# Kernel tuning notes

Hardware: AMD Instinct MI355X
Metric: run time of the kernel (lower is better)

## Reference

```python
import jax, jax.numpy as jnp
import numpy as np

N = 8192
MARGIN = 0.01
PRICE_W = 0.5
RANK_W = 0.5


def setup_inputs() -> dict:
    key = jax.random.key(0)
    k1, k2, k3 = jax.random.split(key, 3)
    predicted_prices = jax.random.normal(k1, (N,), dtype=jnp.float32)
    actual_prices = jax.random.normal(k2, (N,), dtype=jnp.float32)
    # keep previous prices in [0.5, 1.5) so the division is well-behaved
    previous_prices = jax.random.uniform(k3, (N,), dtype=jnp.float32) + 0.5
    return {"predicted_prices": predicted_prices,
            "actual_prices": actual_prices,
            "previous_prices": previous_prices}


def reference(predicted_prices, actual_prices, previous_prices):
    # MSE price loss
    price_loss = jnp.mean((predicted_prices - actual_prices) ** 2)

    pred_r = (predicted_prices - previous_prices) / previous_prices  # [N]
    act_r = (actual_prices - previous_prices) / previous_prices     # [N]

    # pairwise differences (i, j): r[i] - r[j]
    act_diff = act_r[:, None] - act_r[None, :]      # [N, N]
    pred_diff = pred_r[:, None] - pred_r[None, :]   # [N, N]

    n = pred_r.shape[0]
    upper = jnp.triu(jnp.ones((n, n), dtype=bool), k=1)  # j > i
    valid = upper & (act_diff != 0)

    # margin_ranking_loss(x1=pred_diff, x2=0, target=sign(act_diff)):
    #   max(0, -target * pred_diff + margin)
    hinge = jnp.maximum(0.0, -jnp.sign(act_diff) * pred_diff + MARGIN)

    count = jnp.sum(valid)
    rank_sum = jnp.sum(jnp.where(valid, hinge, 0.0))
    ranking_loss = jnp.where(
        count > 0,
        rank_sum / jnp.maximum(count, 1).astype(hinge.dtype),
        jnp.zeros((), dtype=hinge.dtype),
    )

    total_loss = PRICE_W * price_loss + RANK_W * ranking_loss
    return total_loss
```

## Files before the change

kernel.cpp:

```cpp
#include <hip/hip_runtime.h>

constexpr int    NN     = 8192;
constexpr float  MARGIN = 0.01f;
constexpr int    BT     = 256;
constexpr int    FI     = 4;
constexpr int    TI     = BT * FI;
constexpr int    TJ     = 32;
constexpr int    NTI    = NN / TI;
constexpr int    NTJ    = NN / TJ;
constexpr int    NBLOCKS = 8 * 256 - 32 * 28;

__global__ __launch_bounds__(BT)
void pair_kernel(const float* __restrict__ pred,
                 const float* __restrict__ act,
                 const float* __restrict__ prev,
                 double* __restrict__ partials)
{
    int t  = blockIdx.x;
    int ib = 0;
    while (t >= NTJ - 32 * ib) { t -= NTJ - 32 * ib; ++ib; }
    const int  jc        = 32 * ib + t;
    const bool diag_like = (t < 32);
    const bool do_price  = (t == 0);

    __shared__ alignas(16) float2 s_t[TJ];

    const int tid = threadIdx.x;
    if (tid < TJ) {
        const int   j   = jc * TJ + tid;
        const float pv  = prev[j];
        const float rcp = __builtin_amdgcn_rcpf(pv);
        s_t[tid] = make_float2((pred[j] - pv) * rcp, (act[j] - pv) * rcp);
    }

    float pri[FI], ari[FI];
    double pp = 0.0;
#pragma unroll
    for (int f = 0; f < FI; ++f) {
        const int   i   = ib * TI + f * BT + tid;
        const float pv  = prev[i];
        const float p   = pred[i];
        const float a   = act[i];
        const float rcp = __builtin_amdgcn_rcpf(pv);
        pri[f] = (p - pv) * rcp;
        ari[f] = (a - pv) * rcp;
        if (do_price) {
            const float d = p - a;
            pp += (double)(d * d);
        }
    }

    __syncthreads();

    float acc[FI] = {0.f, 0.f, 0.f, 0.f};

#define PAIR(f, pj, aj)                                     \
    {                                                       \
        const float ad = ari[f] - (aj);                     \
        const float pd = pri[f] - (pj);                     \
        const float s  = (ad > 0.0f) ? -1.0f : 1.0f;        \
        acc[f] += fmaxf(0.0f, fmaf(s, pd, MARGIN));         \
    }

    const float4* __restrict__ s4 = (const float4*)s_t;
#pragma unroll
    for (int g = 0; g < TJ / 2; ++g) {
        const float4 q = s4[g];
        PAIR(0, q.x, q.y); PAIR(1, q.x, q.y);
        PAIR(2, q.x, q.y); PAIR(3, q.x, q.y);
        PAIR(0, q.z, q.w); PAIR(1, q.z, q.w);
        PAIR(2, q.z, q.w); PAIR(3, q.z, q.w);
    }
#undef PAIR

    double ws = (double)((acc[0] + acc[1]) + (acc[2] + acc[3]));
    if (!diag_like) ws += ws;

    for (int off = 32; off > 0; off >>= 1) {
        ws += __shfl_down(ws, off, 64);
        pp += __shfl_down(pp, off, 64);
    }

    __shared__ double rs[4], rp[4];
    const int w = tid >> 6;
    if ((tid & 63) == 0) { rs[w] = ws; rp[w] = pp; }
    __syncthreads();
    if (tid == 0) {
        partials[2 * blockIdx.x + 0] = rs[0] + rs[1] + rs[2] + rs[3];
        partials[2 * blockIdx.x + 1] = rp[0] + rp[1] + rp[2] + rp[3];
    }
}

__global__ __launch_bounds__(256)
void finalize_kernel(const double* __restrict__ partials,
                     float* __restrict__ out)
{
    double s = 0.0, p = 0.0;
    for (int t = threadIdx.x; t < NBLOCKS; t += 256) {
        s += partials[2 * t + 0];
        p += partials[2 * t + 1];
    }
    for (int off = 32; off > 0; off >>= 1) {
        s += __shfl_down(s, off, 64);
        p += __shfl_down(p, off, 64);
    }
    __shared__ double rs[4], rp[4];
    const int w = threadIdx.x >> 6;
    if ((threadIdx.x & 63) == 0) { rs[w] = s; rp[w] = p; }
    __syncthreads();
    if (threadIdx.x == 0) {
        const double S = rs[0] + rs[1] + rs[2] + rs[3];
        const double P = rp[0] + rp[1] + rp[2] + rp[3];
        const double rank = (S - (double)NN * (double)MARGIN)
                          / ((double)NN * (double)(NN - 1));
        out[0] = (float)(0.5 * (P / (double)NN) + 0.5 * rank);
    }
}

extern "C" void kernel_launch(void* const* d_in, const int* in_sizes, int n_in,
                              void* d_out, int out_size, void* d_ws, size_t ws_size,
                              hipStream_t stream)
{
    const float* pred = (const float*)d_in[0];
    const float* act  = (const float*)d_in[1];
    const float* prev = (const float*)d_in[2];

    double* partials = (double*)d_ws;

    pair_kernel<<<NBLOCKS, BT, 0, stream>>>(pred, act, prev, partials);
    finalize_kernel<<<1, 256, 0, stream>>>(partials, (float*)d_out);
}
```

Before: 14.75 us.

## Halve rows per thread, double block count, and reduce partials in float

Each thread now covers 2 i-rows instead of 4, so the triangular tiling uses 512-row i-blocks and roughly twice as many blocks, giving more parallelism across the CUs. The double-precision wave-shuffle reductions are replaced by a float shared-memory plus shuffle reduction, and rank and price partials are stored in separate float arrays, with the price partial written once per i-block. Each j-tile value loaded from LDS is now reused across fewer rows, per-block overhead rises, and summing in float may cost some accuracy.

```diff
diff --git a/kernel.cpp b/kernel.cpp
--- a/kernel.cpp
+++ b/kernel.cpp
@@ -3,27 +3,30 @@
 constexpr int    NN     = 8192;
 constexpr float  MARGIN = 0.01f;
 constexpr int    BT     = 256;
-constexpr int    FI     = 4;
+constexpr int    FI     = 2;
 constexpr int    TI     = BT * FI;
 constexpr int    TJ     = 32;
 constexpr int    NTI    = NN / TI;
 constexpr int    NTJ    = NN / TJ;
-constexpr int    NBLOCKS = 8 * 256 - 32 * 28;
+constexpr int    NBLOCKS = 16 * 256 - 16 * 120;
 
 __global__ __launch_bounds__(BT)
 void pair_kernel(const float* __restrict__ pred,
                  const float* __restrict__ act,
                  const float* __restrict__ prev,
-                 double* __restrict__ partials)
+                 float* __restrict__ rank_part,
+                 float* __restrict__ price_part)
 {
     int t  = blockIdx.x;
     int ib = 0;
-    while (t >= NTJ - 32 * ib) { t -= NTJ - 32 * ib; ++ib; }
-    const int  jc        = 32 * ib + t;
-    const bool diag_like = (t < 32);
+    while (t >= NTJ - 16 * ib) { t -= NTJ - 16 * ib; ++ib; }
+    const int  jc        = 16 * ib + t;
+    const bool diag_like = (t < 16);
     const bool do_price  = (t == 0);
 
     __shared__ alignas(16) float2 s_t[TJ];
+    __shared__ float s_red[BT];
+    __shared__ float s_pp[BT];
 
     const int tid = threadIdx.x;
     if (tid < TJ) {
@@ -34,7 +37,7 @@
     }
 
     float pri[FI], ari[FI];
-    double pp = 0.0;
+    float pp = 0.f;
 #pragma unroll
     for (int f = 0; f < FI; ++f) {
         const int   i   = ib * TI + f * BT + tid;
@@ -44,62 +47,58 @@
         const float rcp = __builtin_amdgcn_rcpf(pv);
         pri[f] = (p - pv) * rcp;
         ari[f] = (a - pv) * rcp;
-        if (do_price) {
-            const float d = p - a;
-            pp += (double)(d * d);
-        }
+        const float d = p - a;
+        pp += d * d;
     }
 
     __syncthreads();
 
-    float acc[FI] = {0.f, 0.f, 0.f, 0.f};
+    float acc[4] = {0.f, 0.f, 0.f, 0.f};
 
-#define PAIR(f, pj, aj)                                     \
+#define PAIR(f, k, pj, aj)                                  \
     {                                                       \
         const float ad = ari[f] - (aj);                     \
         const float pd = pri[f] - (pj);                     \
         const float s  = (ad > 0.0f) ? -1.0f : 1.0f;        \
-        acc[f] += fmaxf(0.0f, fmaf(s, pd, MARGIN));         \
+        acc[k] += fmaxf(0.0f, fmaf(s, pd, MARGIN));         \
     }
 
     const float4* __restrict__ s4 = (const float4*)s_t;
 #pragma unroll
     for (int g = 0; g < TJ / 2; ++g) {
         const float4 q = s4[g];
-        PAIR(0, q.x, q.y); PAIR(1, q.x, q.y);
-        PAIR(2, q.x, q.y); PAIR(3, q.x, q.y);
-        PAIR(0, q.z, q.w); PAIR(1, q.z, q.w);
-        PAIR(2, q.z, q.w); PAIR(3, q.z, q.w);
+        PAIR(0, 0, q.x, q.y); PAIR(1, 1, q.x, q.y);
+        PAIR(0, 2, q.z, q.w); PAIR(1, 3, q.z, q.w);
     }
 #undef PAIR
 
-    double ws = (double)((acc[0] + acc[1]) + (acc[2] + acc[3]));
-    if (!diag_like) ws += ws;
+    float w = (acc[0] + acc[1]) + (acc[2] + acc[3]);
+    if (!diag_like) w += w;
 
-    for (int off = 32; off > 0; off >>= 1) {
-        ws += __shfl_down(ws, off, 64);
-        pp += __shfl_down(pp, off, 64);
-    }
+    s_red[tid] = w;
+    s_pp[tid]  = pp;
+    __syncthreads();
 
-    __shared__ double rs[4], rp[4];
-    const int w = tid >> 6;
-    if ((tid & 63) == 0) { rs[w] = ws; rp[w] = pp; }
-    __syncthreads();
-    if (tid == 0) {
-        partials[2 * blockIdx.x + 0] = rs[0] + rs[1] + rs[2] + rs[3];
-        partials[2 * blockIdx.x + 1] = rp[0] + rp[1] + rp[2] + rp[3];
+    if (tid < 64) {
+        float r = s_red[tid] + s_red[tid + 64] + s_red[tid + 128] + s_red[tid + 192];
+        for (int off = 32; off > 0; off >>= 1) r += __shfl_down(r, off, 64);
+        if (tid == 0) rank_part[blockIdx.x] = r;
+        if (do_price) {
+            float q = s_pp[tid] + s_pp[tid + 64] + s_pp[tid + 128] + s_pp[tid + 192];
+            for (int off = 32; off > 0; off >>= 1) q += __shfl_down(q, off, 64);
+            if (tid == 0) price_part[ib] = q;
+        }
     }
 }
 
 __global__ __launch_bounds__(256)
-void finalize_kernel(const double* __restrict__ partials,
+void finalize_kernel(const float* __restrict__ rank_part,
+                     const float* __restrict__ price_part,
                      float* __restrict__ out)
 {
     double s = 0.0, p = 0.0;
-    for (int t = threadIdx.x; t < NBLOCKS; t += 256) {
-        s += partials[2 * t + 0];
-        p += partials[2 * t + 1];
-    }
+    for (int t = threadIdx.x; t < NBLOCKS; t += 256) s += (double)rank_part[t];
+    if (threadIdx.x < NTI) p = (double)price_part[threadIdx.x];
     for (int off = 32; off > 0; off >>= 1) {
         s += __shfl_down(s, off, 64);
         p += __shfl_down(p, off, 64);
@@ -125,8 +124,10 @@
     const float* act  = (const float*)d_in[1];
     const float* prev = (const float*)d_in[2];
 
-    double* partials = (double*)d_ws;
+    char* w = (char*)d_ws;
+    float* rank_part  = (float*)w;
+    float* price_part = (float*)(w + 12288);
 
-    pair_kernel<<<NBLOCKS, BT, 0, stream>>>(pred, act, prev, partials);
-    finalize_kernel<<<1, 256, 0, stream>>>(partials, (float*)d_out);
+    pair_kernel<<<NBLOCKS, BT, 0, stream>>>(pred, act, prev, rank_part, price_part);
+    finalize_kernel<<<1, 256, 0, stream>>>(rank_part, price_part, (float*)d_out);
 }
```

Result: slower. 15.31 us (+3.8%).

## Fuse finalize into pair kernel via last-block atomic counter, widen j tile

Applied to the files above, without the earlier changes.

Drops the separate finalize kernel. Each block writes a float partial and bumps an atomic counter, and the last block to finish does the final reduction. The j-tile grows from 32 to 64, which halves the block count, and per-block partials and the price sum now use float instead of double. A memset of the counter is added before the launch, and float partials may lose some accuracy.

```diff
diff --git a/kernel.cpp b/kernel.cpp
--- a/kernel.cpp
+++ b/kernel.cpp
@@ -1,26 +1,30 @@
 #include <hip/hip_runtime.h>
 
-constexpr int    NN     = 8192;
-constexpr float  MARGIN = 0.01f;
-constexpr int    BT     = 256;
-constexpr int    FI     = 4;
-constexpr int    TI     = BT * FI;
-constexpr int    TJ     = 32;
-constexpr int    NTI    = NN / TI;
-constexpr int    NTJ    = NN / TJ;
-constexpr int    NBLOCKS = 8 * 256 - 32 * 28;
+constexpr int    NN      = 8192;
+constexpr float  MARGIN  = 0.01f;
+constexpr int    BT      = 256;
+constexpr int    FI      = 4;
+constexpr int    TI      = BT * FI;
+constexpr int    TJ      = 64;
+constexpr int    NTI     = NN / TI;
+constexpr int    NTJ     = NN / TJ;
+constexpr int    CPR     = TI / TJ;
+constexpr int    NBLOCKS = NTI * NTJ - CPR * (NTI * (NTI - 1) / 2);
 
 __global__ __launch_bounds__(BT)
 void pair_kernel(const float* __restrict__ pred,
                  const float* __restrict__ act,
                  const float* __restrict__ prev,
-                 double* __restrict__ partials)
+                 unsigned int* __restrict__ counter,
+                 float* __restrict__ rank_part,
+                 float* __restrict__ price_part,
+                 float* __restrict__ out)
 {
     int t  = blockIdx.x;
     int ib = 0;
-    while (t >= NTJ - 32 * ib) { t -= NTJ - 32 * ib; ++ib; }
-    const int  jc        = 32 * ib + t;
-    const bool diag_like = (t < 32);
+    while (t >= NTJ - CPR * ib) { t -= NTJ - CPR * ib; ++ib; }
+    const int  jc        = CPR * ib + t;
+    const bool diag_like = (t < CPR);
     const bool do_price  = (t == 0);
 
     __shared__ alignas(16) float2 s_t[TJ];
@@ -34,7 +38,7 @@
     }
 
     float pri[FI], ari[FI];
-    double pp = 0.0;
+    float pp = 0.f;
 #pragma unroll
     for (int f = 0; f < FI; ++f) {
         const int   i   = ib * TI + f * BT + tid;
@@ -46,7 +50,7 @@
         ari[f] = (a - pv) * rcp;
         if (do_price) {
             const float d = p - a;
-            pp += (double)(d * d);
+            pp += d * d;
         }
     }
 
@@ -73,44 +77,42 @@
     }
 #undef PAIR
 
-    double ws = (double)((acc[0] + acc[1]) + (acc[2] + acc[3]));
-    if (!diag_like) ws += ws;
+    float w = (acc[0] + acc[1]) + (acc[2] + acc[3]);
+    if (!diag_like) w += w;
 
-    for (int off = 32; off > 0; off >>= 1) {
-        ws += __shfl_down(ws, off, 64);
-        pp += __shfl_down(pp, off, 64);
+    for (int off = 32; off > 0; off >>= 1) w += __shfl_down(w, off, 64);
+    __shared__ float r_s[4], r_p[4];
+    __shared__ bool  lastf;
+    if ((tid & 63) == 0) r_s[tid >> 6] = w;
+    if (do_price) {
+        for (int off = 32; off > 0; off >>= 1) pp += __shfl_down(pp, off, 64);
+        if ((tid & 63) == 0) r_p[tid >> 6] = pp;
     }
+    __syncthreads();
 
-    __shared__ double rs[4], rp[4];
-    const int w = tid >> 6;
-    if ((tid & 63) == 0) { rs[w] = ws; rp[w] = pp; }
+    if (tid == 0) {
+        rank_part[blockIdx.x] = r_s[0] + r_s[1] + r_s[2] + r_s[3];
+        if (do_price) price_part[ib] = r_p[0] + r_p[1] + r_p[2] + r_p[3];
+        const unsigned tk = __hip_atomic_fetch_add(counter, 1u, __ATOMIC_ACQ_REL,
+                                                   __HIP_MEMORY_SCOPE_AGENT);
+        lastf = (tk == (unsigned)(NBLOCKS - 1));
+    }
     __syncthreads();
-    if (tid == 0) {
-        partials[2 * blockIdx.x + 0] = rs[0] + rs[1] + rs[2] + rs[3];
-        partials[2 * blockIdx.x + 1] = rp[0] + rp[1] + rp[2] + rp[3];
-    }
-}
+    if (!lastf) return;
 
-__global__ __launch_bounds__(256)
-void finalize_kernel(const double* __restrict__ partials,
-                     float* __restrict__ out)
-{
     double s = 0.0, p = 0.0;
-    for (int t = threadIdx.x; t < NBLOCKS; t += 256) {
-        s += partials[2 * t + 0];
-        p += partials[2 * t + 1];
-    }
+    for (int k = tid; k < NBLOCKS; k += BT) s += (double)rank_part[k];
+    if (tid < NTI) p = (double)price_part[tid];
     for (int off = 32; off > 0; off >>= 1) {
         s += __shfl_down(s, off, 64);
         p += __shfl_down(p, off, 64);
     }
-    __shared__ double rs[4], rp[4];
-    const int w = threadIdx.x >> 6;
-    if ((threadIdx.x & 63) == 0) { rs[w] = s; rp[w] = p; }
+    __shared__ double rs2[4], rp2[4];
+    if ((tid & 63) == 0) { rs2[tid >> 6] = s; rp2[tid >> 6] = p; }
     __syncthreads();
-    if (threadIdx.x == 0) {
-        const double S = rs[0] + rs[1] + rs[2] + rs[3];
-        const double P = rp[0] + rp[1] + rp[2] + rp[3];
+    if (tid == 0) {
+        const double S = rs2[0] + rs2[1] + rs2[2] + rs2[3];
+        const double P = rp2[0] + rp2[1] + rp2[2] + rp2[3];
         const double rank = (S - (double)NN * (double)MARGIN)
                           / ((double)NN * (double)(NN - 1));
         out[0] = (float)(0.5 * (P / (double)NN) + 0.5 * rank);
@@ -125,8 +127,12 @@
     const float* act  = (const float*)d_in[1];
     const float* prev = (const float*)d_in[2];
 
-    double* partials = (double*)d_ws;
+    char* w = (char*)d_ws;
+    unsigned int* counter    = (unsigned int*)(w + 0);
+    float*        price_part = (float*)(w + 64);
+    float*        rank_part  = (float*)(w + 256);
 
-    pair_kernel<<<NBLOCKS, BT, 0, stream>>>(pred, act, prev, partials);
-    finalize_kernel<<<1, 256, 0, stream>>>(partials, (float*)d_out);
+    hipMemsetAsync(counter, 0, 4, stream);
+    pair_kernel<<<NBLOCKS, BT, 0, stream>>>(pred, act, prev, counter,
+                                            rank_part, price_part, (float*)d_out);
 }
```

New measurement: 25.08 us. 1.7x slower.
